# Kernel optimization log

Hardware: AMD Instinct MI355X
Metric: run time of the kernel (lower is better)

## Reference

```python
import jax, jax.numpy as jnp
import numpy as np

B, C, H, W = 16, 512, 32, 32
COND_C, L_COND = 768, 77
N_GROUPS, N_HEADS = 8, 8
HEAD = C // N_HEADS
EPS = 1e-5


def setup_inputs() -> dict:
    key = jax.random.key(0)
    ks = jax.random.split(key, 6)
    s = lambda fan_in: 1.0 / np.sqrt(fan_in)
    return {
        "x_0": jax.random.normal(ks[0], (B, C, H, W), jnp.float32),
        "cond": jax.random.normal(ks[1], (B, L_COND, COND_C), jnp.float32),
        "gn_gamma": jnp.ones((C,), jnp.float32),
        "gn_beta": jnp.zeros((C,), jnp.float32),
        "qkv_w": jax.random.normal(ks[2], (3 * C, C), jnp.float32) * s(C),
        "qkv_b": jnp.zeros((3 * C,), jnp.float32),
        "cond_kv_w": jax.random.normal(ks[3], (2 * C, COND_C), jnp.float32) * s(COND_C),
        "cond_kv_b": jnp.zeros((2 * C,), jnp.float32),
        "out_w": jax.random.normal(ks[4], (C, C), jnp.float32) * s(C),
        "out_b": jnp.zeros((C,), jnp.float32),
    }


def reference(x_0, cond, gn_gamma, gn_beta, qkv_w, qkv_b, cond_kv_w, cond_kv_b, out_w, out_b):
    b, c, h, w = x_0.shape
    L = h * w
    # --- GroupNorm over (C/G, H, W) per group, per-channel affine ---
    xg = x_0.reshape(b, N_GROUPS, c // N_GROUPS, h * w)
    mu = xg.mean(axis=(2, 3), keepdims=True)
    var = xg.var(axis=(2, 3), keepdims=True)
    xn = ((xg - mu) * jax.lax.rsqrt(var + EPS)).reshape(b, c, h, w)
    xn = xn * gn_gamma[None, :, None, None] + gn_beta[None, :, None, None]
    # --- to tokens [B, L, C] ---
    x = xn.transpose(0, 2, 3, 1).reshape(b, L, c)
    # --- QKV ---
    qkv = x @ qkv_w.T + qkv_b  # [B, L, 3C]
    q, k, v = jnp.split(qkv, 3, axis=-1)
    q = q.reshape(b, L, N_HEADS, HEAD)
    k = k.reshape(b, L, N_HEADS, HEAD)
    v = v.reshape(b, L, N_HEADS, HEAD)
    # --- conditional K/V ---
    kv_c = cond @ cond_kv_w.T + cond_kv_b  # [B, Lc, 2C]
    k_c, v_c = jnp.split(kv_c, 2, axis=-1)
    Lc = cond.shape[1]
    k_c = k_c.reshape(b, Lc, N_HEADS, HEAD)
    v_c = v_c.reshape(b, Lc, N_HEADS, HEAD)
    K = jnp.concatenate([k, k_c], axis=1)  # [B, L+Lc, H, D]
    V = jnp.concatenate([v, v_c], axis=1)
    # --- attention (full score matrix, as in the original) ---
    scale = HEAD ** -0.5
    scores = jnp.einsum("bqhd,bkhd->bhqk", q, K) * scale
    att = jax.nn.softmax(scores, axis=-1)
    out = jnp.einsum("bhqk,bkhd->bqhd", att, V).reshape(b, L, c)
    out = out @ out_w.T + out_b
    # --- back to image + residual ---
    out = out.reshape(b, h, w, c).transpose(0, 3, 1, 2)
    return out + x_0
```

## Files before the change

### kernel.cpp

```cpp
#include <hip/hip_runtime.h>

typedef short bf16x8 __attribute__((ext_vector_type(8)));
typedef float f32x4 __attribute__((ext_vector_type(4)));
typedef float f32x16 __attribute__((ext_vector_type(16)));
typedef unsigned int u32x4 __attribute__((ext_vector_type(4)));

#define KVP 1152

__device__ __forceinline__ unsigned short f2b(float f) {
    unsigned int u = __float_as_uint(f);
    u += 0x7FFFu + ((u >> 16) & 1u);
    return (unsigned short)(u >> 16);
}

__device__ __forceinline__ f32x4 mfma16(bf16x8 a, bf16x8 b, f32x4 c) {
    return __builtin_amdgcn_mfma_f32_16x16x32_bf16(a, b, c, 0, 0, 0);
}
__device__ __forceinline__ f32x16 mfma32(bf16x8 a, bf16x8 b, f32x16 c) {
    return __builtin_amdgcn_mfma_f32_32x32x16_bf16(a, b, c, 0, 0, 0);
}
__device__ __forceinline__ float exp2_raw(float x) {
    float r; asm("v_exp_f32 %0, %1" : "=v"(r) : "v"(x)); return r;
}
__device__ __forceinline__ unsigned cvt_pk(float lo, float hi) {
    unsigned r; asm("v_cvt_pk_bf16_f32 %0, %1, %2" : "=v"(r) : "v"(lo), "v"(hi)); return r;
}

typedef __attribute__((address_space(3))) unsigned int lds_u32_t;
typedef const __attribute__((address_space(1))) unsigned int glb_u32_t;
__device__ __forceinline__ void async_cp16(const void* g, void* l) {
    __builtin_amdgcn_global_load_lds((glb_u32_t*)(unsigned long long)g,
                                     (lds_u32_t*)(unsigned int)(unsigned long long)l,
                                     16, 0, 0);
}

__global__ __launch_bounds__(256) void gn_stats_k(const float* __restrict__ x, float* __restrict__ stats) {
    int bg = blockIdx.x;
    const float4* p = (const float4*)(x + (size_t)bg * 64 * 1024);
    float s = 0.f, ss = 0.f;
    for (int i = threadIdx.x; i < 16384; i += 256) {
        float4 v = p[i];
        s  += v.x + v.y + v.z + v.w;
        ss += v.x * v.x + v.y * v.y + v.z * v.z + v.w * v.w;
    }
#pragma unroll
    for (int o = 32; o; o >>= 1) { s += __shfl_down(s, o); ss += __shfl_down(ss, o); }
    __shared__ float red[8];
    int w = threadIdx.x >> 6;
    if ((threadIdx.x & 63) == 0) { red[w] = s; red[4 + w] = ss; }
    __syncthreads();
    if (threadIdx.x == 0) {
        s  = red[0] + red[1] + red[2] + red[3];
        ss = red[4] + red[5] + red[6] + red[7];
        float mean = s * (1.f / 65536.f);
        float var  = ss * (1.f / 65536.f) - mean * mean;
        stats[2 * bg]     = mean;
        stats[2 * bg + 1] = rsqrtf(var + 1e-5f);
    }
}

__global__ __launch_bounds__(256) void gn_apply_k(const float* __restrict__ x, const float* __restrict__ stats,
                                                  const float* __restrict__ gamma, const float* __restrict__ beta,
                                                  unsigned short* __restrict__ xt) {
    int st = blockIdx.x & 15;
    int ct = (blockIdx.x >> 4) & 7;
    int b  = blockIdx.x >> 7;
    float mean = stats[2 * (b * 8 + ct)];
    float rsig = stats[2 * (b * 8 + ct) + 1];
    __shared__ unsigned short tile[64][65];
    int tid = threadIdx.x;
#pragma unroll
    for (int it = 0; it < 4; ++it) {
        int idx = it * 256 + tid;
        int ci = idx >> 4, j4 = idx & 15;
        int c = ct * 64 + ci;
        float4 v = *(const float4*)(x + ((size_t)b * 512 + c) * 1024 + st * 64 + j4 * 4);
        float gs = gamma[c] * rsig;
        float bo = beta[c] - mean * gs;
        tile[j4 * 4 + 0][ci] = f2b(v.x * gs + bo);
        tile[j4 * 4 + 1][ci] = f2b(v.y * gs + bo);
        tile[j4 * 4 + 2][ci] = f2b(v.z * gs + bo);
        tile[j4 * 4 + 3][ci] = f2b(v.w * gs + bo);
    }
    __syncthreads();
#pragma unroll
    for (int it = 0; it < 4; ++it) {
        int idx = it * 256 + tid;
        int si = idx >> 4, q = idx & 15;
        uint2 u;
        u.x = (unsigned)tile[si][q * 4 + 0] | ((unsigned)tile[si][q * 4 + 1] << 16);
        u.y = (unsigned)tile[si][q * 4 + 2] | ((unsigned)tile[si][q * 4 + 3] << 16);
        *(uint2*)(xt + ((size_t)b * 1024 + st * 64 + si) * 512 + ct * 64 + q * 4) = u;
    }
}

__global__ __launch_bounds__(256) void cvt_k(const float* __restrict__ in, unsigned short* __restrict__ out, int n4) {
    int i = blockIdx.x * 256 + threadIdx.x;
    if (i < n4) {
        float4 v = ((const float4*)in)[i];
        uint2 u;
        u.x = (unsigned)f2b(v.x) | ((unsigned)f2b(v.y) << 16);
        u.y = (unsigned)f2b(v.z) | ((unsigned)f2b(v.w) << 16);
        ((uint2*)out)[i] = u;
    }
}

template <int EPI>
__global__ __launch_bounds__(256) void gemm128_k(const unsigned short* __restrict__ A,
                                                 const unsigned short* __restrict__ Bw,
                                                 const float* __restrict__ bias,
                                                 int M, int N, int K,
                                                 unsigned short* __restrict__ Qo,
                                                 unsigned short* __restrict__ Ko,
                                                 unsigned short* __restrict__ Vo,
                                                 const float* __restrict__ x0,
                                                 float* __restrict__ outp) {
    __shared__ __align__(16) unsigned short As[128 * 32];
    __shared__ __align__(16) unsigned short Bs[128 * 32];
    const int m0 = blockIdx.x * 128, n0 = blockIdx.y * 128;
    const int tid = threadIdx.x, lane = tid & 63, w = tid >> 6;
    const int wr = w >> 1, wc = w & 1;
    const int lc = lane & 15, lg = lane >> 4;

    const int sRow = lane >> 2;
    const int sSlot = (lane & 3) ^ ((lane >> 3) & 3);
    const unsigned short* aSrc0 = A + (size_t)(m0 + 16 * w + sRow) * K + sSlot * 8;
    const unsigned short* aSrc1 = A + (size_t)(m0 + 64 + 16 * w + sRow) * K + sSlot * 8;
    const unsigned short* bSrc0 = Bw + (size_t)(n0 + 16 * w + sRow) * K + sSlot * 8;
    const unsigned short* bSrc1 = Bw + (size_t)(n0 + 64 + 16 * w + sRow) * K + sSlot * 8;
    unsigned short* aDst0 = As + (size_t)w * 512;
    unsigned short* aDst1 = As + (size_t)(4 + w) * 512;
    unsigned short* bDst0 = Bs + (size_t)w * 512;
    unsigned short* bDst1 = Bs + (size_t)(4 + w) * 512;

    const int rSlot8 = (lg ^ ((lc >> 1) & 3)) * 8;

    f32x4 acc[4][4];
#pragma unroll
    for (int m = 0; m < 4; ++m)
#pragma unroll
        for (int n = 0; n < 4; ++n) acc[m][n] = (f32x4){0.f, 0.f, 0.f, 0.f};

    for (int k0 = 0; k0 < K; k0 += 32) {
        async_cp16(aSrc0 + k0, aDst0);
        async_cp16(aSrc1 + k0, aDst1);
        async_cp16(bSrc0 + k0, bDst0);
        async_cp16(bSrc1 + k0, bDst1);
        __syncthreads();
        bf16x8 af[4], bfr[4];
#pragma unroll
        for (int m = 0; m < 4; ++m)
            af[m] = *(const bf16x8*)&As[(wr * 64 + m * 16 + lc) * 32 + rSlot8];
#pragma unroll
        for (int n = 0; n < 4; ++n)
            bfr[n] = *(const bf16x8*)&Bs[(wc * 64 + n * 16 + lc) * 32 + rSlot8];
#pragma unroll
        for (int m = 0; m < 4; ++m)
#pragma unroll
            for (int n = 0; n < 4; ++n)
                acc[m][n] = mfma16(af[m], bfr[n], acc[m][n]);
        __syncthreads();
    }

#pragma unroll
    for (int n = 0; n < 4; ++n) {
        int col = n0 + wc * 64 + n * 16 + lc;
        float bv = bias[col];
#pragma unroll
        for (int m = 0; m < 4; ++m) {
            int rb = m0 + wr * 64 + m * 16 + lg * 4;
#pragma unroll
            for (int r = 0; r < 4; ++r) {
                int token = rb + r;
                float val = acc[m][n][r] + bv;
                if (EPI == 0) {
                    int b = token >> 10, l = token & 1023;
                    if (col < 512) {
                        int hh = col >> 6, d = col & 63;
                        Qo[((size_t)(b * 8 + hh) * 1024 + l) * 64 + d] = f2b(val * (0.125f * 1.44269504089f));
                    } else if (col < 1024) {
                        int j = col - 512, hh = j >> 6, d = j & 63;
                        Ko[((size_t)(b * 8 + hh) * KVP + l) * 64 + d] = f2b(val);
                    } else {
                        int j = col - 1024, hh = j >> 6, d = j & 63;
                        Vo[((size_t)(b * 8 + hh) * 64 + d) * KVP + l] = f2b(val);
                    }
                } else {
                    int b = token >> 10, hw = token & 1023;
                    size_t a = ((size_t)b * 512 + col) * 1024 + hw;
                    outp[a] = val + x0[a];
                }
            }
        }
    }
}

__global__ __launch_bounds__(256) void gemm_nt_k(const unsigned short* __restrict__ A,
                                                 const unsigned short* __restrict__ Bw,
                                                 const float* __restrict__ bias,
                                                 int M, int N, int K,
                                                 unsigned short* __restrict__ Ko,
                                                 unsigned short* __restrict__ Vo) {
    __shared__ unsigned short As[64][40];
    __shared__ unsigned short Bs[64][40];
    const int m0 = blockIdx.x * 64, n0 = blockIdx.y * 64;
    const int tid = threadIdx.x, lane = tid & 63, w = tid >> 6;
    const int lc = lane & 15, lg = lane >> 4;
    const int lrow = tid >> 2, lseg = tid & 3;
    f32x4 acc[4];
#pragma unroll
    for (int i = 0; i < 4; ++i) acc[i] = (f32x4){0.f, 0.f, 0.f, 0.f};

    for (int k0 = 0; k0 < K; k0 += 32) {
        uint4 av = make_uint4(0u, 0u, 0u, 0u);
        if (m0 + lrow < M) av = *(const uint4*)(A + (size_t)(m0 + lrow) * K + k0 + lseg * 8);
        *(uint4*)&As[lrow][lseg * 8] = av;
        uint4 bv = *(const uint4*)(Bw + (size_t)(n0 + lrow) * K + k0 + lseg * 8);
        *(uint4*)&Bs[lrow][lseg * 8] = bv;
        __syncthreads();
        bf16x8 af = *(const bf16x8*)&As[w * 16 + lc][lg * 8];
#pragma unroll
        for (int ct = 0; ct < 4; ++ct) {
            bf16x8 bfr = *(const bf16x8*)&Bs[ct * 16 + lc][lg * 8];
            acc[ct] = mfma16(af, bfr, acc[ct]);
        }
        __syncthreads();
    }

    const int rbase = m0 + w * 16 + lg * 4;
#pragma unroll
    for (int ct = 0; ct < 4; ++ct) {
        int col = n0 + ct * 16 + lc;
        float bv = bias[col];
#pragma unroll
        for (int r = 0; r < 4; ++r) {
            int token = rbase + r;
            if (token >= M) continue;
            float val = acc[ct][r] + bv;
            int b = token / 77, l = token - b * 77;
            if (col < 512) {
                int hh = col >> 6, d = col & 63;
                Ko[((size_t)(b * 8 + hh) * KVP + 1024 + l) * 64 + d] = f2b(val);
            } else {
                int j = col - 512, hh = j >> 6, d = j & 63;
                Vo[((size_t)(b * 8 + hh) * 64 + d) * KVP + 1024 + l] = f2b(val);
            }
        }
    }
}

__global__ __launch_bounds__(512) void attn2_k(const unsigned short* __restrict__ Q,
                                               const unsigned short* __restrict__ Kb,
                                               const unsigned short* __restrict__ Vt,
                                               unsigned short* __restrict__ atok) {
    __shared__ __align__(16) unsigned short lds[18432];

    const int bh = blockIdx.x >> 2;
    const int qt = blockIdx.x & 3;
    const int w  = threadIdx.x >> 6;
    const int lane = threadIdx.x & 63;
    const int ql = lane & 31, hi = lane >> 5;
    const int q0 = qt * 256 + w * 32;

    bf16x8 qf[4];
    const unsigned short* Qp = Q + ((size_t)bh * 1024 + q0 + ql) * 64 + hi * 8;
#pragma unroll
    for (int ks = 0; ks < 4; ++ks) qf[ks] = *(const bf16x8*)(Qp + ks * 16);

    const unsigned short* Kg = Kb + (size_t)bh * KVP * 64;
    const unsigned short* Vg = Vt + (size_t)bh * 64 * KVP;

    const int srow = lane >> 3;
    const int sc   = (((lane & 7) ^ (lane >> 3)) << 3);

    f32x16 o0, o1;
#pragma unroll
    for (int i = 0; i < 16; ++i) { o0[i] = 0.f; o1[i] = 0.f; }
    float mreg = -1e30f, lsum = 0.f;

    {
        uint4 kr = *(const uint4*)(Kg + (size_t)(8 * w + srow) * 64 + sc);
        uint4 vr = *(const uint4*)(Vg + (size_t)(8 * w + srow) * KVP + sc);
        *(uint4*)&lds[w * 512 + lane * 8] = kr;
        *(uint4*)&lds[4096 + w * 512 + lane * 8] = vr;
    }
    __syncthreads();

    int cur = 0;
    for (int it = 0; it < 18; ++it) {
        const int kv0 = it * 64;
        const bool pre = (it < 17);
        uint4 kn, vn;
        if (pre) {
            kn = *(const uint4*)(Kg + (size_t)(kv0 + 64 + 8 * w + srow) * 64 + sc);
            vn = *(const uint4*)(Vg + (size_t)(8 * w + srow) * KVP + kv0 + 64 + sc);
        }
        const int kb = cur * 8192, vb = cur * 8192 + 4096;

        f32x16 s0, s1;
#pragma unroll
        for (int i = 0; i < 16; ++i) { s0[i] = 0.f; s1[i] = 0.f; }
#pragma unroll
        for (int ks = 0; ks < 4; ++ks) {
            const int sl = ((ks * 2 + hi) ^ (ql & 7)) << 3;
            bf16x8 kf0 = *(const bf16x8*)&lds[kb + ql * 64 + sl];
            bf16x8 kf1 = *(const bf16x8*)&lds[kb + (32 + ql) * 64 + sl];
            s0 = mfma32(kf0, qf[ks], s0);
            s1 = mfma32(kf1, qf[ks], s1);
        }
        if (kv0 == 1088) {
#pragma unroll
            for (int r = 0; r < 16; ++r) {
                int kva = 1088 + (r & 3) + 8 * (r >> 2) + 4 * hi;
                if (kva >= 1101) s0[r] = -1e30f;
                if (kva + 32 >= 1101) s1[r] = -1e30f;
            }
        }

        float t[16];
#pragma unroll
        for (int i = 0; i < 16; ++i) t[i] = fmaxf(s0[i], s1[i]);
#pragma unroll
        for (int st = 8; st; st >>= 1)
#pragma unroll
            for (int i = 0; i < st; ++i) t[i] = fmaxf(t[i], t[i + st]);
        float pmax = fmaxf(t[0], __shfl_xor(t[0], 32));

        if (__any(pmax > mreg + 8.f)) {
            float mn = fmaxf(mreg, pmax);
            float al = exp2_raw(mreg - mn);
            mreg = mn;
            lsum *= al;
#pragma unroll
            for (int i = 0; i < 16; ++i) { o0[i] *= al; o1[i] *= al; }
        }

        unsigned pk0[8], pk1[8];
        float sA = 0.f, sB = 0.f, sC = 0.f, sD = 0.f;
#pragma unroll
        for (int i = 0; i < 8; ++i) {
            float a0 = exp2_raw(s0[2 * i] - mreg), a1 = exp2_raw(s0[2 * i + 1] - mreg);
            float b0 = exp2_raw(s1[2 * i] - mreg), b1 = exp2_raw(s1[2 * i + 1] - mreg);
            pk0[i] = cvt_pk(a0, a1);
            pk1[i] = cvt_pk(b0, b1);
            sA += a0; sB += a1; sC += b0; sD += b1;
        }
        float ls = (sA + sB) + (sC + sD);
        ls += __shfl_xor(ls, 32);
        lsum += ls;

#pragma unroll
        for (int t2 = 0; t2 < 2; ++t2) {
            const unsigned* pk = t2 ? pk1 : pk0;
#pragma unroll
            for (int v = 0; v < 2; ++v) {
                unsigned a0 = pk[4 * v], a1 = pk[4 * v + 1], a2 = pk[4 * v + 2], a3 = pk[4 * v + 3];
                unsigned x = __shfl_xor(hi ? a0 : a2, 32);
                unsigned y = __shfl_xor(hi ? a1 : a3, 32);
                u32x4 fw;
                fw.x = hi ? x : a0; fw.y = hi ? y : a1; fw.z = hi ? a2 : x; fw.w = hi ? a3 : y;
                bf16x8 pf = __builtin_bit_cast(bf16x8, fw);
                const int ks2 = 2 * t2 + v;
                const int sl = ((ks2 * 2 + hi) ^ (ql & 7)) << 3;
                bf16x8 vf0 = *(const bf16x8*)&lds[vb + ql * 64 + sl];
                bf16x8 vf1 = *(const bf16x8*)&lds[vb + (32 + ql) * 64 + sl];
                o0 = mfma32(vf0, pf, o0);
                o1 = mfma32(vf1, pf, o1);
            }
        }

        if (pre) {
            *(uint4*)&lds[(cur ^ 1) * 8192 + w * 512 + lane * 8] = kn;
            *(uint4*)&lds[(cur ^ 1) * 8192 + 4096 + w * 512 + lane * 8] = vn;
        }
        __syncthreads();
        cur ^= 1;
    }

    float rinv = 1.f / lsum;
    unsigned short* sw = &lds[w * 2304];
#pragma unroll
    for (int dt = 0; dt < 2; ++dt) {
#pragma unroll
        for (int rp = 0; rp < 8; ++rp) {
            float e0 = (dt ? o1[2 * rp] : o0[2 * rp]) * rinv;
            float e1 = (dt ? o1[2 * rp + 1] : o0[2 * rp + 1]) * rinv;
            int d = dt * 32 + ((2 * rp) & 3) + 8 * ((2 * rp) >> 2) + 4 * hi;
            *(unsigned*)&sw[ql * 72 + d] = cvt_pk(e0, e1);
        }
    }
    __syncthreads();
    {
        int i = threadIdx.x >> 1, hf = threadIdx.x & 1;
        const unsigned short* src = &lds[(i >> 5) * 2304 + (i & 31) * 72 + hf * 32];
        u32x4 r0 = *(const u32x4*)(src);
        u32x4 r1 = *(const u32x4*)(src + 8);
        u32x4 r2 = *(const u32x4*)(src + 16);
        u32x4 r3 = *(const u32x4*)(src + 24);
        int b = bh >> 3, h = bh & 7;
        unsigned short* gd = atok + ((size_t)b * 1024 + qt * 256 + i) * 512 + h * 64 + hf * 32;
        *(u32x4*)(gd) = r0;
        *(u32x4*)(gd + 8) = r1;
        *(u32x4*)(gd + 16) = r2;
        *(u32x4*)(gd + 24) = r3;
    }
}

extern "C" void kernel_launch(void* const* d_in, const int* in_sizes, int n_in,
                              void* d_out, int out_size, void* d_ws, size_t ws_size,
                              hipStream_t stream) {
    const float* x0     = (const float*)d_in[0];
    const float* cond   = (const float*)d_in[1];
    const float* gamma  = (const float*)d_in[2];
    const float* beta   = (const float*)d_in[3];
    const float* qkv_w  = (const float*)d_in[4];
    const float* qkv_b  = (const float*)d_in[5];
    const float* ckv_w  = (const float*)d_in[6];
    const float* ckv_b  = (const float*)d_in[7];
    const float* out_w  = (const float*)d_in[8];
    const float* out_b  = (const float*)d_in[9];
    float* outp = (float*)d_out;

    char* p = (char*)d_ws;
    float* stats = (float*)p;            p += 1024;
    unsigned short* xt    = (unsigned short*)p; p += (size_t)16384 * 512 * 2;
    unsigned short* wqkv  = (unsigned short*)p; p += (size_t)1536 * 512 * 2;
    unsigned short* wckv  = (unsigned short*)p; p += (size_t)1024 * 768 * 2;
    unsigned short* wout  = (unsigned short*)p; p += (size_t)512 * 512 * 2;
    unsigned short* condb = (unsigned short*)p; p += (size_t)1232 * 768 * 2;
    unsigned short* Qb    = (unsigned short*)p; p += (size_t)16 * 8 * 1024 * 64 * 2;
    unsigned short* Kb    = (unsigned short*)p; p += (size_t)16 * 8 * KVP * 64 * 2;
    unsigned short* Vtb   = (unsigned short*)p; p += (size_t)16 * 8 * KVP * 64 * 2;
    unsigned short* atok  = (unsigned short*)p; p += (size_t)16384 * 512 * 2;

    gn_stats_k<<<128, 256, 0, stream>>>(x0, stats);
    gn_apply_k<<<2048, 256, 0, stream>>>(x0, stats, gamma, beta, xt);
    cvt_k<<<768, 256, 0, stream>>>(qkv_w, wqkv, 196608);
    cvt_k<<<768, 256, 0, stream>>>(ckv_w, wckv, 196608);
    cvt_k<<<256, 256, 0, stream>>>(out_w, wout, 65536);
    cvt_k<<<924, 256, 0, stream>>>(cond, condb, 236544);

    gemm128_k<0><<<dim3(128, 12), 256, 0, stream>>>(xt, wqkv, qkv_b, 16384, 1536, 512,
                                                    Qb, Kb, Vtb, nullptr, nullptr);
    gemm_nt_k<<<dim3(20, 16), 256, 0, stream>>>(condb, wckv, ckv_b, 1232, 1024, 768, Kb, Vtb);
    attn2_k<<<512, 512, 0, stream>>>(Qb, Kb, Vtb, atok);
    gemm128_k<2><<<dim3(128, 4), 256, 0, stream>>>(atok, wout, out_b, 16384, 512, 512,
                                                   nullptr, nullptr, nullptr, x0, outp);
}
```

Before: 195.4 us.

## Double-buffer LDS tiles in gemm128 to overlap loads with MFMA

Splits the A and B shared-memory tiles into two buffers and issues the async copies for the next K-slice before running the MFMAs on the current one. This aims to hide global-to-LDS load latency behind matrix math, where before every K-step waited on its own load. In exchange it doubles the GEMM kernel's LDS use, which may lower occupancy, and it relies on the existing end-of-loop barrier to order the buffer reuse.

```diff
diff --git a/kernel.cpp b/kernel.cpp
--- a/kernel.cpp
+++ b/kernel.cpp
@@ -115,8 +115,8 @@
                                                  unsigned short* __restrict__ Vo,
                                                  const float* __restrict__ x0,
                                                  float* __restrict__ outp) {
-    __shared__ __align__(16) unsigned short As[128 * 32];
-    __shared__ __align__(16) unsigned short Bs[128 * 32];
+    __shared__ __align__(16) unsigned short As[2][4096];
+    __shared__ __align__(16) unsigned short Bs[2][4096];
     const int m0 = blockIdx.x * 128, n0 = blockIdx.y * 128;
     const int tid = threadIdx.x, lane = tid & 63, w = tid >> 6;
     const int wr = w >> 1, wc = w & 1;
@@ -128,10 +128,6 @@
     const unsigned short* aSrc1 = A + (size_t)(m0 + 64 + 16 * w + sRow) * K + sSlot * 8;
     const unsigned short* bSrc0 = Bw + (size_t)(n0 + 16 * w + sRow) * K + sSlot * 8;
     const unsigned short* bSrc1 = Bw + (size_t)(n0 + 64 + 16 * w + sRow) * K + sSlot * 8;
-    unsigned short* aDst0 = As + (size_t)w * 512;
-    unsigned short* aDst1 = As + (size_t)(4 + w) * 512;
-    unsigned short* bDst0 = Bs + (size_t)w * 512;
-    unsigned short* bDst1 = Bs + (size_t)(4 + w) * 512;
 
     const int rSlot8 = (lg ^ ((lc >> 1) & 3)) * 8;
 
@@ -141,19 +137,31 @@
 #pragma unroll
         for (int n = 0; n < 4; ++n) acc[m][n] = (f32x4){0.f, 0.f, 0.f, 0.f};
 
-    for (int k0 = 0; k0 < K; k0 += 32) {
-        async_cp16(aSrc0 + k0, aDst0);
-        async_cp16(aSrc1 + k0, aDst1);
-        async_cp16(bSrc0 + k0, bDst0);
-        async_cp16(bSrc1 + k0, bDst1);
-        __syncthreads();
+    const int nT = K >> 5;
+    {
+        async_cp16(aSrc0, &As[0][w * 512]);
+        async_cp16(aSrc1, &As[0][(4 + w) * 512]);
+        async_cp16(bSrc0, &Bs[0][w * 512]);
+        async_cp16(bSrc1, &Bs[0][(4 + w) * 512]);
+    }
+    __syncthreads();
+
+    for (int t = 0; t < nT; ++t) {
+        const int cur = t & 1;
+        if (t + 1 < nT) {
+            const int k1 = (t + 1) << 5;
+            async_cp16(aSrc0 + k1, &As[cur ^ 1][w * 512]);
+            async_cp16(aSrc1 + k1, &As[cur ^ 1][(4 + w) * 512]);
+            async_cp16(bSrc0 + k1, &Bs[cur ^ 1][w * 512]);
+            async_cp16(bSrc1 + k1, &Bs[cur ^ 1][(4 + w) * 512]);
+        }
         bf16x8 af[4], bfr[4];
 #pragma unroll
         for (int m = 0; m < 4; ++m)
-            af[m] = *(const bf16x8*)&As[(wr * 64 + m * 16 + lc) * 32 + rSlot8];
+            af[m] = *(const bf16x8*)&As[cur][(wr * 64 + m * 16 + lc) * 32 + rSlot8];
 #pragma unroll
         for (int n = 0; n < 4; ++n)
-            bfr[n] = *(const bf16x8*)&Bs[(wc * 64 + n * 16 + lc) * 32 + rSlot8];
+            bfr[n] = *(const bf16x8*)&Bs[cur][(wc * 64 + n * 16 + lc) * 32 + rSlot8];
 #pragma unroll
         for (int m = 0; m < 4; ++m)
 #pragma unroll
```

New measurement: 195.5 us. Within noise of the previous version (+0.0%).
